# Performance work log

Measured on AMD Instinct MI355X. Metric: run time of the kernel, lower is better.

## Reference

```python
import jax, jax.numpy as jnp
import numpy as np

N_NODES = 100000
N_EDGES = 1600000
D_IN = 128
D_OUT = 5


def setup_inputs() -> dict:
    key = jax.random.key(0)
    k1, k2, k3, k4, k5 = jax.random.split(key, 5)
    x = jax.random.normal(k1, (N_NODES, D_IN), dtype=jnp.float32)
    edge_index = jax.random.randint(k2, (2, N_EDGES), 0, N_NODES, dtype=jnp.int64)
    scale = 1.0 / np.sqrt(D_IN)
    W_l = jax.random.normal(k3, (D_OUT, D_IN), dtype=jnp.float32) * scale
    b_l = jax.random.normal(k4, (D_OUT,), dtype=jnp.float32) * scale
    W_r = jax.random.normal(k5, (D_OUT, D_IN), dtype=jnp.float32) * scale
    return {"x": x, "edge_index": edge_index, "W_l": W_l, "b_l": b_l, "W_r": W_r}


def reference(x, edge_index, W_l, b_l, W_r):
    # PyG SAGEConv with aggr='mean', root_weight=True:
    # out_i = mean_{j: (j->i) in E} x_j @ W_l^T + b_l + x_i @ W_r^T
    n = x.shape[0]
    src = edge_index[0]
    dst = edge_index[1]
    msgs = x[src]  # [E, D_in] gather (irregular access)
    agg_sum = jax.ops.segment_sum(msgs, dst, num_segments=n)  # [N, D_in]
    deg = jax.ops.segment_sum(jnp.ones(src.shape, dtype=x.dtype), dst, num_segments=n)
    agg_mean = agg_sum / jnp.maximum(deg, 1.0)[:, None]  # zero-degree nodes -> 0
    out = agg_mean @ W_l.T + b_l + x @ W_r.T  # [N, D_out]
    return out
```

## Files before the change

### kernel.cpp

```cpp
#include <hip/hip_runtime.h>
#include <hip/hip_fp16.h>


#define N_NODES 100000
#define N_EDGES 1600000
#define D_IN 128

#define HR_STRIDE 8
#define N_PAD 100352

#define B_NODES 196
#define N_BUCKETS 512
#define CAP 3840

#define SC_EPT 8
#define SC_EPB (256 * SC_EPT)
#define SC_GRID ((N_EDGES + SC_EPB - 1) / SC_EPB)

#define PROJ_NPB 128
#define PROJ_BLOCKS ((N_NODES + PROJ_NPB - 1) / PROJ_NPB)

typedef unsigned long long u64;
typedef unsigned int u32;

__device__ __forceinline__ float dot8(const float4 a0, const float4 a1,
                                      const float4 b0, const float4 b1) {
    return a0.x * b0.x + a0.y * b0.y + a0.z * b0.z + a0.w * b0.w
         + a1.x * b1.x + a1.y * b1.y + a1.z * b1.z + a1.w * b1.w;
}

__global__ __launch_bounds__(256, 4) void proj_kernel(
    const float* __restrict__ x,
    const float* __restrict__ Wl,
    const float* __restrict__ Wr,
    uint4* __restrict__ hl,
    float* __restrict__ hr)
{
    __shared__ __align__(16) char xb[4][2][4096];

    const int tid  = threadIdx.x;
    const int wvi  = tid >> 6;
    const int lane = tid & 63;
    const int g    = lane >> 4;
    const int k    = lane & 15;

    const int wnode0 = blockIdx.x * PROJ_NPB + wvi * 32;
    const char* xbytes = (const char*)x;
    const size_t XLIM = (size_t)N_NODES * 512 - 16;

    float4 wv[10][2];
#pragma unroll
    for (int o = 0; o < 10; ++o) {
        const float* w = (o < 5 ? Wl + o * D_IN : Wr + (o - 5) * D_IN) + k * 8;
        wv[o][0] = ((const float4*)w)[0];
        wv[o][1] = ((const float4*)w)[1];
    }

#define PSTAGE(bufi, batch)                                                  \
    {                                                                        \
        const size_t gb0 = (size_t)(wnode0 + (batch) * 8) * 512;             \
        _Pragma("unroll")                                                    \
        for (int r = 0; r < 4; ++r) {                                        \
            const int loff = r * 1024 + lane * 16;                           \
            size_t goff = gb0 + (size_t)loff;                                \
            goff = goff > XLIM ? XLIM : goff;                                \
            __builtin_amdgcn_global_load_lds(                                \
                (const __attribute__((address_space(1))) void*)(xbytes + goff), \
                (__attribute__((address_space(3))) void*)(&xb[wvi][bufi][loff]), \
                16, 0, 0);                                                   \
        }                                                                    \
    }

    PSTAGE(0, 0);
    PSTAGE(1, 1);

#pragma unroll
    for (int b = 0; b < 4; ++b) {
        if (b == 3) asm volatile("s_waitcnt vmcnt(0)" ::: "memory");
        else        asm volatile("s_waitcnt vmcnt(4)" ::: "memory");

        const char* xc = &xb[wvi][b & 1][0];
#pragma unroll
        for (int u = 0; u < 2; ++u) {
            const int nlb  = g * 2 + u;
            const int node = wnode0 + b * 8 + nlb;
            const float4* xp = (const float4*)(xc + nlb * 512 + k * 32);
            float4 x0 = xp[0];
            float4 x1 = xp[1];

            float s[10];
#pragma unroll
            for (int o = 0; o < 10; ++o)
                s[o] = dot8(x0, x1, wv[o][0], wv[o][1]);

#pragma unroll
            for (int o = 0; o < 10; ++o) {
                s[o] += __shfl_xor(s[o], 8, 64);
                s[o] += __shfl_xor(s[o], 4, 64);
                s[o] += __shfl_xor(s[o], 2, 64);
                s[o] += __shfl_xor(s[o], 1, 64);
            }

            if (k == 0) {
                u32 u0 = (u32)__half_as_ushort(__float2half_rn(s[0]));
                u32 u1 = (u32)__half_as_ushort(__float2half_rn(s[1]));
                u32 u2 = (u32)__half_as_ushort(__float2half_rn(s[2]));
                u32 u3 = (u32)__half_as_ushort(__float2half_rn(s[3]));
                u32 u4 = (u32)__half_as_ushort(__float2half_rn(s[4]));
                uint4 pk;
                pk.x = u0 | (u1 << 16);
                pk.y = u2 | (u3 << 16);
                pk.z = u4;
                pk.w = 0u;
                hl[node] = pk;

                float* pr = hr + (size_t)node * HR_STRIDE;
                *(float4*)pr = make_float4(s[5], s[6], s[7], s[8]);
                pr[4] = s[9];
            }
        }
        if (b < 2) {
            asm volatile("s_waitcnt lgkmcnt(0)" ::: "memory");
            PSTAGE(b & 1, b + 2);
        }
    }
#undef PSTAGE
}

__global__ __launch_bounds__(256) void scatter_kernel(
    const int* __restrict__ ei,
    u32* __restrict__ sorted,
    int* __restrict__ cursor)
{
    __shared__ int hist[N_BUCKETS];
    __shared__ int basepos[N_BUCKETS];

    const int tid = threadIdx.x;
    for (int i = tid; i < N_BUCKETS; i += 256) hist[i] = 0;
    __syncthreads();

    const int e0 = blockIdx.x * SC_EPB + tid * SC_EPT;

    int srcv[SC_EPT], dstv[SC_EPT], slot[SC_EPT];
    bool valid[SC_EPT];

    if (e0 + SC_EPT <= N_EDGES) {
        const int4* s4 = (const int4*)(ei + e0);
        const int4* d4 = (const int4*)(ei + N_EDGES + e0);
#pragma unroll
        for (int c = 0; c < SC_EPT / 4; ++c) {
            int4 sv = s4[c], dv = d4[c];
            srcv[c*4+0] = sv.x; srcv[c*4+1] = sv.y;
            srcv[c*4+2] = sv.z; srcv[c*4+3] = sv.w;
            dstv[c*4+0] = dv.x; dstv[c*4+1] = dv.y;
            dstv[c*4+2] = dv.z; dstv[c*4+3] = dv.w;
        }
#pragma unroll
        for (int q = 0; q < SC_EPT; ++q) valid[q] = true;
    } else {
#pragma unroll
        for (int q = 0; q < SC_EPT; ++q) {
            int e = e0 + q;
            valid[q] = (e < N_EDGES);
            srcv[q] = valid[q] ? ei[e] : 0;
            dstv[q] = valid[q] ? ei[N_EDGES + e] : 0;
        }
    }

#pragma unroll
    for (int q = 0; q < SC_EPT; ++q) {
        if (valid[q]) {
            unsigned b = (unsigned)dstv[q] / 196u;
            slot[q] = atomicAdd(&hist[b], 1);
        }
    }
    __syncthreads();

    for (int b = tid; b < N_BUCKETS; b += 256) {
        int c = hist[b];
        if (c > 0) basepos[b] = atomicAdd(&cursor[b], c);
    }
    __syncthreads();

#pragma unroll
    for (int q = 0; q < SC_EPT; ++q) {
        if (valid[q]) {
            unsigned b = (unsigned)dstv[q] / 196u;
            unsigned r = (unsigned)dstv[q] - b * 196u;
            sorted[(size_t)b * CAP + basepos[b] + slot[q]] =
                (r << 17) | (unsigned)srcv[q];
        }
    }
}

#define AGG_T 512

__global__ __launch_bounds__(512) void agg_kernel(
    const u32* __restrict__ sorted,
    const int* __restrict__ cursor,
    const uint4* __restrict__ hl,
    const float* __restrict__ hr,
    const float* __restrict__ bias,
    float* __restrict__ out)
{
    __shared__ u32 hist[B_NODES];
    __shared__ u32 deg[B_NODES];
    __shared__ u32 offs[B_NODES];
    __shared__ u32 srcs[CAP];
    __shared__ float part[B_NODES][5];

    const int b   = blockIdx.x;
    const int tid = threadIdx.x;

    for (int i = tid; i < B_NODES; i += AGG_T) hist[i] = 0u;
    __syncthreads();

    const int cnt = min(cursor[b], CAP);
    const u32* sp = sorted + (size_t)b * CAP;

    u32 ev[8];
    int rv[8], sl[8];
#pragma unroll
    for (int q = 0; q < 8; ++q) {
        int i = tid + q * AGG_T;
        ev[q] = (i < cnt) ? sp[i] : 0xFFFFFFFFu;
    }
#pragma unroll
    for (int q = 0; q < 8; ++q) {
        if (ev[q] != 0xFFFFFFFFu) {
            rv[q] = (int)(ev[q] >> 17);
            sl[q] = (int)atomicAdd(&hist[rv[q]], 1u);
        }
    }
    __syncthreads();

    if (tid < B_NODES) { deg[tid] = hist[tid]; offs[tid] = hist[tid]; }
    __syncthreads();
#pragma unroll
    for (int s = 1; s < B_NODES; s <<= 1) {
        u32 v = 0;
        if (tid < B_NODES && tid >= s) v = offs[tid - s];
        __syncthreads();
        if (tid < B_NODES) offs[tid] += v;
        __syncthreads();
    }
    if (tid < B_NODES) offs[tid] -= deg[tid];
    __syncthreads();

#pragma unroll
    for (int q = 0; q < 8; ++q) {
        if (ev[q] != 0xFFFFFFFFu)
            srcs[offs[rv[q]] + (u32)sl[q]] = ev[q] & 0x1FFFFu;
    }
    __syncthreads();

    float a0 = 0.f, a1 = 0.f, a2 = 0.f, a3 = 0.f, a4 = 0.f;
    if (tid < 2 * B_NODES) {
        const int p = (tid >= B_NODES);
        const int n = p ? tid - B_NODES : tid;
        const u32 d = deg[n];
        const u32 o = offs[n];
        const u32 h0 = (d + 1) >> 1;
        const u32 i0 = p ? o + h0 : o;
        const u32 i1 = p ? o + d : o + h0;
        for (u32 i = i0; i < i1; ++i) {
            u32 s = srcs[i];
            uint4 h = hl[s];
            a0 += __half2float(__ushort_as_half((unsigned short)(h.x & 0xFFFFu)));
            a1 += __half2float(__ushort_as_half((unsigned short)(h.x >> 16)));
            a2 += __half2float(__ushort_as_half((unsigned short)(h.y & 0xFFFFu)));
            a3 += __half2float(__ushort_as_half((unsigned short)(h.y >> 16)));
            a4 += __half2float(__ushort_as_half((unsigned short)(h.z & 0xFFFFu)));
        }
        if (p) {
            part[n][0] = a0; part[n][1] = a1; part[n][2] = a2;
            part[n][3] = a3; part[n][4] = a4;
        }
    }
    __syncthreads();

    if (tid < B_NODES) {
        const int node = b * B_NODES + tid;
        if (node < N_NODES) {
            a0 += part[tid][0]; a1 += part[tid][1]; a2 += part[tid][2];
            a3 += part[tid][3]; a4 += part[tid][4];
            const float rec = 1.0f / fmaxf((float)deg[tid], 1.0f);
            const float* h = hr + (size_t)node * HR_STRIDE;
            float* o = out + (size_t)node * 5;
            o[0] = a0 * rec + bias[0] + h[0];
            o[1] = a1 * rec + bias[1] + h[1];
            o[2] = a2 * rec + bias[2] + h[2];
            o[3] = a3 * rec + bias[3] + h[3];
            o[4] = a4 * rec + bias[4] + h[4];
        }
    }
}

extern "C" void kernel_launch(void* const* d_in, const int* in_sizes, int n_in,
                              void* d_out, int out_size, void* d_ws, size_t ws_size,
                              hipStream_t stream) {
    const float* x    = (const float*)d_in[0];
    const int*   ei   = (const int*)d_in[1];
    const float* Wl   = (const float*)d_in[2];
    const float* bl   = (const float*)d_in[3];
    const float* Wr   = (const float*)d_in[4];
    float*       out  = (float*)d_out;

    uint4* hl     = (uint4*)d_ws;
    float* hr     = (float*)(hl + N_PAD);
    u32*   sorted = (u32*)(hr + (size_t)N_PAD * HR_STRIDE);
    int*   cursor = (int*)(sorted + (size_t)N_BUCKETS * CAP);

    hipMemsetAsync(cursor, 0, N_BUCKETS * sizeof(int), stream);

    proj_kernel<<<PROJ_BLOCKS, 256, 0, stream>>>(x, Wl, Wr, hl, hr);
    scatter_kernel<<<SC_GRID, 256, 0, stream>>>(ei, sorted, cursor);
    agg_kernel<<<N_BUCKETS, 512, 0, stream>>>(sorted, cursor, hl, hr, bl, out);
}
```

Before: 153.7 us.

## Fuse projection and edge scatter into one interleaved-role kernel launch

The projection and bucket-scatter kernels are merged into one launch. Block IDs are interleaved so two of every three blocks do projection and the third scatters edges, letting the x-streaming projection run alongside the edge bucketing and removing one kernel boundary. The projection drops its LDS async-copy double buffer for direct global loads, and processes W_l and W_r in two passes to keep register use down. Edges per scatter thread go from 8 to 16 so the scatter block count is exactly half the projection block count. Risks are losing the latency hiding the LDS pipeline gave and mixing two kernels with different resource needs in one launch.

```diff
diff --git a/kernel.cpp b/kernel.cpp
--- a/kernel.cpp
+++ b/kernel.cpp
@@ -13,12 +13,13 @@
 #define N_BUCKETS 512
 #define CAP 3840
 
-#define SC_EPT 8
+#define SC_EPT 16
 #define SC_EPB (256 * SC_EPT)
 #define SC_GRID ((N_EDGES + SC_EPB - 1) / SC_EPB)
 
 #define PROJ_NPB 128
 #define PROJ_BLOCKS ((N_NODES + PROJ_NPB - 1) / PROJ_NPB)
+#define FUSED_GRID (PROJ_BLOCKS + SC_GRID)
 
 typedef unsigned long long u64;
 typedef unsigned int u32;
@@ -29,166 +30,165 @@
          + a1.x * b1.x + a1.y * b1.y + a1.z * b1.z + a1.w * b1.w;
 }
 
-__global__ __launch_bounds__(256, 4) void proj_kernel(
+__global__ __launch_bounds__(256, 4) void proj_scatter_kernel(
     const float* __restrict__ x,
     const float* __restrict__ Wl,
     const float* __restrict__ Wr,
     uint4* __restrict__ hl,
-    float* __restrict__ hr)
-{
-    __shared__ __align__(16) char xb[4][2][4096];
-
-    const int tid  = threadIdx.x;
-    const int wvi  = tid >> 6;
-    const int lane = tid & 63;
-    const int g    = lane >> 4;
-    const int k    = lane & 15;
-
-    const int wnode0 = blockIdx.x * PROJ_NPB + wvi * 32;
-    const char* xbytes = (const char*)x;
-    const size_t XLIM = (size_t)N_NODES * 512 - 16;
-
-    float4 wv[10][2];
-#pragma unroll
-    for (int o = 0; o < 10; ++o) {
-        const float* w = (o < 5 ? Wl + o * D_IN : Wr + (o - 5) * D_IN) + k * 8;
-        wv[o][0] = ((const float4*)w)[0];
-        wv[o][1] = ((const float4*)w)[1];
-    }
-
-#define PSTAGE(bufi, batch)                                                  \
-    {                                                                        \
-        const size_t gb0 = (size_t)(wnode0 + (batch) * 8) * 512;             \
-        _Pragma("unroll")                                                    \
-        for (int r = 0; r < 4; ++r) {                                        \
-            const int loff = r * 1024 + lane * 16;                           \
-            size_t goff = gb0 + (size_t)loff;                                \
-            goff = goff > XLIM ? XLIM : goff;                                \
-            __builtin_amdgcn_global_load_lds(                                \
-                (const __attribute__((address_space(1))) void*)(xbytes + goff), \
-                (__attribute__((address_space(3))) void*)(&xb[wvi][bufi][loff]), \
-                16, 0, 0);                                                   \
-        }                                                                    \
-    }
-
-    PSTAGE(0, 0);
-    PSTAGE(1, 1);
-
-#pragma unroll
-    for (int b = 0; b < 4; ++b) {
-        if (b == 3) asm volatile("s_waitcnt vmcnt(0)" ::: "memory");
-        else        asm volatile("s_waitcnt vmcnt(4)" ::: "memory");
-
-        const char* xc = &xb[wvi][b & 1][0];
-#pragma unroll
-        for (int u = 0; u < 2; ++u) {
-            const int nlb  = g * 2 + u;
-            const int node = wnode0 + b * 8 + nlb;
-            const float4* xp = (const float4*)(xc + nlb * 512 + k * 32);
-            float4 x0 = xp[0];
-            float4 x1 = xp[1];
-
-            float s[10];
-#pragma unroll
-            for (int o = 0; o < 10; ++o)
-                s[o] = dot8(x0, x1, wv[o][0], wv[o][1]);
-
-#pragma unroll
-            for (int o = 0; o < 10; ++o) {
-                s[o] += __shfl_xor(s[o], 8, 64);
-                s[o] += __shfl_xor(s[o], 4, 64);
-                s[o] += __shfl_xor(s[o], 2, 64);
-                s[o] += __shfl_xor(s[o], 1, 64);
-            }
-
-            if (k == 0) {
-                u32 u0 = (u32)__half_as_ushort(__float2half_rn(s[0]));
-                u32 u1 = (u32)__half_as_ushort(__float2half_rn(s[1]));
-                u32 u2 = (u32)__half_as_ushort(__float2half_rn(s[2]));
-                u32 u3 = (u32)__half_as_ushort(__float2half_rn(s[3]));
-                u32 u4 = (u32)__half_as_ushort(__float2half_rn(s[4]));
-                uint4 pk;
-                pk.x = u0 | (u1 << 16);
-                pk.y = u2 | (u3 << 16);
-                pk.z = u4;
-                pk.w = 0u;
-                hl[node] = pk;
-
-                float* pr = hr + (size_t)node * HR_STRIDE;
-                *(float4*)pr = make_float4(s[5], s[6], s[7], s[8]);
-                pr[4] = s[9];
-            }
-        }
-        if (b < 2) {
-            asm volatile("s_waitcnt lgkmcnt(0)" ::: "memory");
-            PSTAGE(b & 1, b + 2);
-        }
-    }
-#undef PSTAGE
-}
-
-__global__ __launch_bounds__(256) void scatter_kernel(
+    float* __restrict__ hr,
     const int* __restrict__ ei,
     u32* __restrict__ sorted,
     int* __restrict__ cursor)
 {
-    __shared__ int hist[N_BUCKETS];
-    __shared__ int basepos[N_BUCKETS];
-
     const int tid = threadIdx.x;
-    for (int i = tid; i < N_BUCKETS; i += 256) hist[i] = 0;
-    __syncthreads();
-
-    const int e0 = blockIdx.x * SC_EPB + tid * SC_EPT;
-
-    int srcv[SC_EPT], dstv[SC_EPT], slot[SC_EPT];
-    bool valid[SC_EPT];
-
-    if (e0 + SC_EPT <= N_EDGES) {
-        const int4* s4 = (const int4*)(ei + e0);
-        const int4* d4 = (const int4*)(ei + N_EDGES + e0);
-#pragma unroll
-        for (int c = 0; c < SC_EPT / 4; ++c) {
-            int4 sv = s4[c], dv = d4[c];
-            srcv[c*4+0] = sv.x; srcv[c*4+1] = sv.y;
-            srcv[c*4+2] = sv.z; srcv[c*4+3] = sv.w;
-            dstv[c*4+0] = dv.x; dstv[c*4+1] = dv.y;
-            dstv[c*4+2] = dv.z; dstv[c*4+3] = dv.w;
-        }
-#pragma unroll
-        for (int q = 0; q < SC_EPT; ++q) valid[q] = true;
+    const int m   = blockIdx.x % 3;
+    const int d   = blockIdx.x / 3;
+
+    if (m < 2) {
+        const int pidx = d * 2 + m;
+        const int g = tid >> 4;
+        const int k = tid & 15;
+        const int node0 = pidx * PROJ_NPB + g * 8;
+
+#pragma unroll
+        for (int hb = 0; hb < 2; ++hb) {
+            const int nb = node0 + hb * 4;
+
+            float4 xv[4][2];
+            int nodes[4];
+#pragma unroll
+            for (int it = 0; it < 4; ++it) {
+                nodes[it] = min(nb + it, N_NODES - 1);
+                const float4* xr =
+                    (const float4*)(x + (size_t)nodes[it] * D_IN + k * 8);
+                xv[it][0] = xr[0];
+                xv[it][1] = xr[1];
+            }
+
+            {
+                float4 wv[5][2];
+#pragma unroll
+                for (int o = 0; o < 5; ++o) {
+                    const float* w = Wl + o * D_IN + k * 8;
+                    wv[o][0] = ((const float4*)w)[0];
+                    wv[o][1] = ((const float4*)w)[1];
+                }
+#pragma unroll
+                for (int it = 0; it < 4; ++it) {
+                    float s[5];
+#pragma unroll
+                    for (int o = 0; o < 5; ++o)
+                        s[o] = dot8(xv[it][0], xv[it][1], wv[o][0], wv[o][1]);
+#pragma unroll
+                    for (int o = 0; o < 5; ++o) {
+                        s[o] += __shfl_xor(s[o], 8, 64);
+                        s[o] += __shfl_xor(s[o], 4, 64);
+                        s[o] += __shfl_xor(s[o], 2, 64);
+                        s[o] += __shfl_xor(s[o], 1, 64);
+                    }
+                    if (k == 0) {
+                        u32 u0 = (u32)__half_as_ushort(__float2half_rn(s[0]));
+                        u32 u1 = (u32)__half_as_ushort(__float2half_rn(s[1]));
+                        u32 u2 = (u32)__half_as_ushort(__float2half_rn(s[2]));
+                        u32 u3 = (u32)__half_as_ushort(__float2half_rn(s[3]));
+                        u32 u4 = (u32)__half_as_ushort(__float2half_rn(s[4]));
+                        uint4 pk;
+                        pk.x = u0 | (u1 << 16);
+                        pk.y = u2 | (u3 << 16);
+                        pk.z = u4;
+                        pk.w = 0u;
+                        hl[nodes[it]] = pk;
+                    }
+                }
+            }
+
+            {
+                float4 wv[5][2];
+#pragma unroll
+                for (int o = 0; o < 5; ++o) {
+                    const float* w = Wr + o * D_IN + k * 8;
+                    wv[o][0] = ((const float4*)w)[0];
+                    wv[o][1] = ((const float4*)w)[1];
+                }
+#pragma unroll
+                for (int it = 0; it < 4; ++it) {
+                    float s[5];
+#pragma unroll
+                    for (int o = 0; o < 5; ++o)
+                        s[o] = dot8(xv[it][0], xv[it][1], wv[o][0], wv[o][1]);
+#pragma unroll
+                    for (int o = 0; o < 5; ++o) {
+                        s[o] += __shfl_xor(s[o], 8, 64);
+                        s[o] += __shfl_xor(s[o], 4, 64);
+                        s[o] += __shfl_xor(s[o], 2, 64);
+                        s[o] += __shfl_xor(s[o], 1, 64);
+                    }
+                    if (k == 0) {
+                        float* pr = hr + (size_t)nodes[it] * HR_STRIDE;
+                        *(float4*)pr = make_float4(s[0], s[1], s[2], s[3]);
+                        pr[4] = s[4];
+                    }
+                }
+            }
+        }
     } else {
+        __shared__ int hist[N_BUCKETS];
+        __shared__ int basepos[N_BUCKETS];
+
+        for (int i = tid; i < N_BUCKETS; i += 256) hist[i] = 0;
+        __syncthreads();
+
+        const int e0 = d * SC_EPB + tid * SC_EPT;
+
+        int srcv[SC_EPT], dstv[SC_EPT], slot[SC_EPT];
+        bool valid[SC_EPT];
+
+        if (e0 + SC_EPT <= N_EDGES) {
+            const int4* s4 = (const int4*)(ei + e0);
+            const int4* d4 = (const int4*)(ei + N_EDGES + e0);
+#pragma unroll
+            for (int c = 0; c < SC_EPT / 4; ++c) {
+                int4 sv = s4[c], dv = d4[c];
+                srcv[c*4+0] = sv.x; srcv[c*4+1] = sv.y;
+                srcv[c*4+2] = sv.z; srcv[c*4+3] = sv.w;
+                dstv[c*4+0] = dv.x; dstv[c*4+1] = dv.y;
+                dstv[c*4+2] = dv.z; dstv[c*4+3] = dv.w;
+            }
+#pragma unroll
+            for (int q = 0; q < SC_EPT; ++q) valid[q] = true;
+        } else {
+#pragma unroll
+            for (int q = 0; q < SC_EPT; ++q) {
+                int e = e0 + q;
+                valid[q] = (e < N_EDGES);
+                srcv[q] = valid[q] ? ei[e] : 0;
+                dstv[q] = valid[q] ? ei[N_EDGES + e] : 0;
+            }
+        }
+
 #pragma unroll
         for (int q = 0; q < SC_EPT; ++q) {
-            int e = e0 + q;
-            valid[q] = (e < N_EDGES);
-            srcv[q] = valid[q] ? ei[e] : 0;
-            dstv[q] = valid[q] ? ei[N_EDGES + e] : 0;
-        }
-    }
-
-#pragma unroll
-    for (int q = 0; q < SC_EPT; ++q) {
-        if (valid[q]) {
-            unsigned b = (unsigned)dstv[q] / 196u;
-            slot[q] = atomicAdd(&hist[b], 1);
-        }
-    }
-    __syncthreads();
-
-    for (int b = tid; b < N_BUCKETS; b += 256) {
-        int c = hist[b];
-        if (c > 0) basepos[b] = atomicAdd(&cursor[b], c);
-    }
-    __syncthreads();
-
-#pragma unroll
-    for (int q = 0; q < SC_EPT; ++q) {
-        if (valid[q]) {
-            unsigned b = (unsigned)dstv[q] / 196u;
-            unsigned r = (unsigned)dstv[q] - b * 196u;
-            sorted[(size_t)b * CAP + basepos[b] + slot[q]] =
-                (r << 17) | (unsigned)srcv[q];
+            if (valid[q]) {
+                unsigned b = (unsigned)dstv[q] / 196u;
+                slot[q] = atomicAdd(&hist[b], 1);
+            }
+        }
+        __syncthreads();
+
+        for (int b = tid; b < N_BUCKETS; b += 256) {
+            int c = hist[b];
+            if (c > 0) basepos[b] = atomicAdd(&cursor[b], c);
+        }
+        __syncthreads();
+
+#pragma unroll
+        for (int q = 0; q < SC_EPT; ++q) {
+            if (valid[q]) {
+                unsigned b = (unsigned)dstv[q] / 196u;
+                unsigned r = (unsigned)dstv[q] - b * 196u;
+                sorted[(size_t)b * CAP + basepos[b] + slot[q]] =
+                    (r << 17) | (unsigned)srcv[q];
+            }
         }
     }
 }
@@ -313,7 +313,8 @@
 
     hipMemsetAsync(cursor, 0, N_BUCKETS * sizeof(int), stream);
 
-    proj_kernel<<<PROJ_BLOCKS, 256, 0, stream>>>(x, Wl, Wr, hl, hr);
-    scatter_kernel<<<SC_GRID, 256, 0, stream>>>(ei, sorted, cursor);
+    proj_scatter_kernel<<<FUSED_GRID, 256, 0, stream>>>(
+        x, Wl, Wr, hl, hr, ei, sorted, cursor);
+
     agg_kernel<<<N_BUCKETS, 512, 0, stream>>>(sorted, cursor, hl, hr, bl, out);
 }
```

Result: faster. 131.8 us (-14.3%).
